# Optimization experiments

Measured on AMD Instinct MI355X. Metric: run time of the kernel, lower is better.

Reference implementation:

```python
import jax, jax.numpy as jnp
import numpy as np

N_NODES = 50000
N_EDGES = 800000
D_IN = 128
H1 = 128
H2 = 64
N_CLASSES = 4


def _sage_conv(x, src, dst, w_l, w_r, b, num_nodes):
    # PyG SAGEConv (aggr='mean'): out = lin_l(mean_{j->i} x_j) + lin_r(x_i)
    ones = jnp.ones((src.shape[0],), dtype=x.dtype)
    deg = jax.ops.segment_sum(ones, dst, num_segments=num_nodes)  # [N]
    agg = jax.ops.segment_sum(x[src], dst, num_segments=num_nodes)  # [N, d]
    agg = agg / jnp.maximum(deg, 1.0)[:, None]
    return agg @ w_l + b + x @ w_r


def setup_inputs() -> dict:
    key = jax.random.key(0)
    ks = jax.random.split(key, 12)
    x_content = jax.random.normal(ks[0], (N_NODES, D_IN), dtype=jnp.float32)
    edge_index = jax.random.randint(ks[1], (2, N_EDGES), 0, N_NODES, dtype=jnp.int32)
    edge_type = jax.random.randint(ks[2], (N_EDGES,), 0, 4, dtype=jnp.int32)
    s = 0.05
    params = {
        'w_l0': jax.random.normal(ks[3], (D_IN, H1), jnp.float32) * s,
        'w_r0': jax.random.normal(ks[4], (D_IN, H1), jnp.float32) * s,
        'b0': jnp.zeros((H1,), jnp.float32),
        'w_l1': jax.random.normal(ks[5], (H1, H1), jnp.float32) * s,
        'w_r1': jax.random.normal(ks[6], (H1, H1), jnp.float32) * s,
        'b1': jnp.zeros((H1,), jnp.float32),
        'w_l2': jax.random.normal(ks[7], (H1, H2), jnp.float32) * s,
        'w_r2': jax.random.normal(ks[8], (H1, H2), jnp.float32) * s,
        'b2': jnp.zeros((H2,), jnp.float32),
        'w_out': jax.random.normal(ks[9], (H2, N_CLASSES), jnp.float32) * s,
        'b_out': jnp.zeros((N_CLASSES,), jnp.float32),
    }
    return {'x_content': x_content, 'edge_index': edge_index, 'edge_type': edge_type, **params}


def reference(x_content, edge_index, edge_type,
              w_l0, w_r0, b0, w_l1, w_r1, b1, w_l2, w_r2, b2, w_out, b_out):
    # eval mode: dropout is identity
    src, dst = edge_index[0], edge_index[1]
    n = x_content.shape[0]
    x = x_content
    for (wl, wr, b) in ((w_l0, w_r0, b0), (w_l1, w_r1, b1), (w_l2, w_r2, b2)):
        x = _sage_conv(x, src, dst, wl, wr, b, n)
        x = jax.nn.relu(x)
    return x @ w_out + b_out
```

## Files before the change

### kernel.cpp

```cpp
#include <hip/hip_runtime.h>
#include <hip/hip_fp16.h>

#define D 128

constexpr int RSH = 14;
constexpr int RSZ = 1 << RSH;
constexpr int NRANGE = 4;
constexpr int CSH = 15;
constexpr int CSZ = 1 << CSH;

using short8 = __attribute__((ext_vector_type(8))) short;
using f32x4 = __attribute__((ext_vector_type(4))) float;

__device__ inline void splitf(float v, unsigned short& h, unsigned short& l) {
    unsigned b = __float_as_uint(v);
    h = (unsigned short)(b >> 16);
    float fh = __uint_as_float(b & 0xffff0000u);
    float r = v - fh;
    l = (unsigned short)(__float_as_uint(r) >> 16);
}


__global__ __launch_bounds__(1024) void hist_rank(
    const int* __restrict__ dst, unsigned* __restrict__ hist,
    unsigned short* __restrict__ rank, int n_edges, int nchunk) {
    __shared__ unsigned lh[RSZ / 2];
    int b = blockIdx.x;
    int r = b & (NRANGE - 1), c = b >> 2;
    int t = threadIdx.x;
    for (int i = t; i < RSZ / 2; i += 1024) lh[i] = 0;
    __syncthreads();
    int e0 = c << CSH, e1 = min(n_edges, e0 + CSZ);
    for (int e = e0 + t; e < e1; e += 1024) {
        int d = dst[e];
        if ((d >> RSH) == r) {
            int ii = d & (RSZ - 1);
            unsigned sh = (ii & 1) * 16;
            unsigned old = atomicAdd(&lh[ii >> 1], 1u << sh);
            rank[e] = (unsigned short)((old >> sh) & 0xffffu);
        }
    }
    __syncthreads();
    unsigned* gh = hist + (size_t)(r * nchunk + c) * (RSZ / 2);
    for (int i = t; i < RSZ / 2; i += 1024) gh[i] = lh[i];
}

struct WSplitArgs {
    const float* src[6];
    unsigned short* dh[6];
    unsigned short* dl[6];
};

__global__ __launch_bounds__(256) void deg_splitw(
    const unsigned short* __restrict__ hist16, int* __restrict__ deg,
    int* __restrict__ partials, int n_nodes, int nchunk, int nblk, WSplitArgs a) {
    __shared__ int sd[256];
    int b = blockIdx.x, t = threadIdx.x;
    if (b >= nblk) {
        int g = (b - nblk) * 256 + t;
        int m, e, N;
        if (g < 65536) { m = g >> 14; e = g & 16383; N = 128; }
        else { int t2 = g - 65536; m = 4 + (t2 >> 13); e = t2 & 8191; N = 64; }
        int sh = (N == 128) ? 7 : 6;
        int k = e >> sh;
        int n = e & (N - 1);
        float v = a.src[m][e];
        unsigned short h, l;
        splitf(v, h, l);
        a.dh[m][n * 128 + k] = h;
        a.dl[m][n * 128 + k] = l;
        return;
    }
    int i = b * 256 + t;
    int s = 0;
    if (i < n_nodes) {
        int r = i >> RSH, ii = i & (RSZ - 1);
        const unsigned short* hp = hist16 + (size_t)r * nchunk * RSZ + ii;
        for (int c = 0; c < nchunk; ++c) s += hp[(size_t)c * RSZ];
        deg[i] = s;
    }
    sd[t] = s;
    __syncthreads();
    for (int st = 128; st > 0; st >>= 1) {
        if (t < st) sd[t] += sd[t + st];
        __syncthreads();
    }
    if (t == 0) partials[b] = sd[0];
}

__global__ __launch_bounds__(256) void scan_fill(
    const int* __restrict__ deg, const int* __restrict__ partials,
    const unsigned short* __restrict__ hist16, int* __restrict__ row_ptr,
    float* __restrict__ inv_deg, int* __restrict__ base,
    int n_nodes, int nchunk, int nblk) {
    __shared__ int sp[256];
    __shared__ int sd[256];
    int b = blockIdx.x, t = threadIdx.x;

    sp[t] = (t < b && t < nblk) ? partials[t] : 0;
    __syncthreads();
    for (int st = 128; st > 0; st >>= 1) {
        if (t < st) sp[t] += sp[t + st];
        __syncthreads();
    }
    int pbase = sp[0];

    int i = b * 256 + t;
    int v = (i < n_nodes) ? deg[i] : 0;
    sd[t] = v;
    __syncthreads();
    for (int d = 1; d < 256; d <<= 1) {
        int x = (t >= d) ? sd[t - d] : 0;
        __syncthreads();
        sd[t] += x;
        __syncthreads();
    }
    int excl = sd[t] - v + pbase;
    if (i < n_nodes) {
        row_ptr[i] = excl;
        int dv = v > 1 ? v : 1;
        inv_deg[i] = 1.0f / (float)dv;
        if (i == n_nodes - 1) row_ptr[n_nodes] = excl + v;
        int r = i >> RSH, ii = i & (RSZ - 1);
        int bacc = excl;
        for (int c = 0; c < nchunk; ++c) {
            size_t idx = (size_t)(r * nchunk + c) * RSZ + ii;
            base[idx] = bacc;
            bacc += hist16[idx];
        }
    }
}

__global__ __launch_bounds__(256) void fill_edges(
    const int* __restrict__ src, const int* __restrict__ dst,
    const unsigned short* __restrict__ rank, const int* __restrict__ base,
    int* __restrict__ csr, int n_edges, int nchunk) {
    int e = blockIdx.x * 256 + threadIdx.x;
    if (e >= n_edges) return;
    int d = dst[e];
    int c = e >> CSH;
    int r = d >> RSH;
    int slot = base[(size_t)(r * nchunk + c) * RSZ + (d & (RSZ - 1))] + rank[e];
    csr[slot] = src[e];
}

template <int BN, int NT, bool SPLITX>
__global__ __launch_bounds__(256) void gemm_lds(
    const float* __restrict__ X,
    const unsigned short* __restrict__ Ah, const unsigned short* __restrict__ Al,
    const unsigned short* __restrict__ W1h, const unsigned short* __restrict__ W1l,
    const unsigned short* __restrict__ W2h, const unsigned short* __restrict__ W2l,
    const float* __restrict__ bias, __half* __restrict__ P, float* __restrict__ Q, int M) {
    __shared__ short8 As[2][16 * 65];

    const int tid = threadIdx.x;
    const int wave = tid >> 6;
    const int lane = tid & 63;
    const int l15 = lane & 15;
    const int q = lane >> 4;
    const int m0 = blockIdx.x * 64;

    if constexpr (SPLITX) {
#pragma unroll
        for (int it = 0; it < 4; ++it) {
            int s = it * 256 + tid;
            int row = s >> 4, col16 = s & 15;
            int gr = min(m0 + row, M - 1);
            const float4* xp = (const float4*)X + (size_t)gr * 32 + col16 * 2;
            float4 v0 = xp[0], v1 = xp[1];
            float fv[8] = {v0.x, v0.y, v0.z, v0.w, v1.x, v1.y, v1.z, v1.w};
            short8 h, l;
#pragma unroll
            for (int j = 0; j < 8; ++j) {
                unsigned short hh_, ll_;
                splitf(fv[j], hh_, ll_);
                h[j] = (short)hh_;
                l[j] = (short)ll_;
            }
            As[0][col16 * 65 + row] = h;
            As[1][col16 * 65 + row] = l;
        }
    } else {
#pragma unroll
        for (int it = 0; it < 8; ++it) {
            int s = it * 256 + tid;
            int arr = s >> 10;
            int sp = s & 1023;
            int row = sp >> 4, col16 = sp & 15;
            int gr = min(m0 + row, M - 1);
            const unsigned short* src = (arr ? Al : Ah) + (size_t)gr * 128 + col16 * 8;
            As[arr][col16 * 65 + row] = *(const short8*)src;
        }
    }
    __syncthreads();

    const int isQ = wave >> 1;
    const int colbase = (wave & 1) * (NT * 16);
    const unsigned short* Wh = isQ ? W2h : W1h;
    const unsigned short* Wl = isQ ? W2l : W1l;

    float bvs[NT];
#pragma unroll
    for (int nt = 0; nt < NT; ++nt) bvs[nt] = isQ ? bias[colbase + nt * 16 + l15] : 0.f;

    f32x4 acc[4][NT] = {};

#pragma unroll 1
    for (int kt = 0; kt < 4; ++kt) {
        short8 Bh[NT], Bl[NT];
#pragma unroll
        for (int nt = 0; nt < NT; ++nt) {
            int c = colbase + nt * 16 + l15;
            int off = c * 128 + kt * 32 + q * 8;
            Bh[nt] = *(const short8*)(Wh + off);
            Bl[nt] = *(const short8*)(Wl + off);
        }
#pragma unroll
        for (int mt = 0; mt < 4; ++mt) {
            int ai = (kt * 4 + q) * 65 + mt * 16 + l15;
            short8 Afh = As[0][ai];
            short8 Afl = As[1][ai];
#pragma unroll
            for (int nt = 0; nt < NT; ++nt) {
                acc[mt][nt] = __builtin_amdgcn_mfma_f32_16x16x32_bf16(Afh, Bh[nt], acc[mt][nt], 0, 0, 0);
                acc[mt][nt] = __builtin_amdgcn_mfma_f32_16x16x32_bf16(Afh, Bl[nt], acc[mt][nt], 0, 0, 0);
                acc[mt][nt] = __builtin_amdgcn_mfma_f32_16x16x32_bf16(Afl, Bh[nt], acc[mt][nt], 0, 0, 0);
            }
        }
    }

#pragma unroll
    for (int mt = 0; mt < 4; ++mt) {
        int orow = m0 + mt * 16 + q * 4;
#pragma unroll
        for (int nt = 0; nt < NT; ++nt) {
            int col = colbase + nt * 16 + l15;
#pragma unroll
            for (int r = 0; r < 4; ++r) {
                int rr = orow + r;
                if (rr < M) {
                    if (isQ) Q[(size_t)rr * BN + col] = acc[mt][nt][r] + bvs[nt];
                    else P[(size_t)rr * BN + col] = __float2half(acc[mt][nt][r]);
                }
            }
        }
    }
}

__global__ __launch_bounds__(256) void agg_fused128(
    const __half* __restrict__ P, const float* __restrict__ Q,
    const int* __restrict__ row_ptr, const int* __restrict__ csr,
    const float* __restrict__ inv_deg, unsigned short* __restrict__ Hh,
    unsigned short* __restrict__ Hl, int n_nodes) {
    int node = (blockIdx.x * blockDim.x + threadIdx.x) >> 6;
    int lane = threadIdx.x & 63;
    if (node >= n_nodes) return;
    int beg = row_ptr[node], end = row_ptr[node + 1];
    const int g = lane >> 4;
    const int l = lane & 15;
    float a[2][8] = {};
    int e = beg;
    for (; e + 8 <= end; e += 8) {
#pragma unroll
        for (int j = 0; j < 2; ++j) {
            int s = csr[e + 4 * j + g];
            uint4 raw = *(const uint4*)(P + (size_t)s * 128 + l * 8);
            float2 f01 = __half22float2(*reinterpret_cast<__half2*>(&raw.x));
            float2 f23 = __half22float2(*reinterpret_cast<__half2*>(&raw.y));
            float2 f45 = __half22float2(*reinterpret_cast<__half2*>(&raw.z));
            float2 f67 = __half22float2(*reinterpret_cast<__half2*>(&raw.w));
            a[j][0] += f01.x; a[j][1] += f01.y; a[j][2] += f23.x; a[j][3] += f23.y;
            a[j][4] += f45.x; a[j][5] += f45.y; a[j][6] += f67.x; a[j][7] += f67.y;
        }
    }
    for (; e < end; e += 4) {
        int idx = e + g;
        if (idx < end) {
            int s = csr[idx];
            uint4 raw = *(const uint4*)(P + (size_t)s * 128 + l * 8);
            float2 f01 = __half22float2(*reinterpret_cast<__half2*>(&raw.x));
            float2 f23 = __half22float2(*reinterpret_cast<__half2*>(&raw.y));
            float2 f45 = __half22float2(*reinterpret_cast<__half2*>(&raw.z));
            float2 f67 = __half22float2(*reinterpret_cast<__half2*>(&raw.w));
            a[0][0] += f01.x; a[0][1] += f01.y; a[0][2] += f23.x; a[0][3] += f23.y;
            a[0][4] += f45.x; a[0][5] += f45.y; a[0][6] += f67.x; a[0][7] += f67.y;
        }
    }
    float s[8];
#pragma unroll
    for (int k = 0; k < 8; ++k) {
        s[k] = a[0][k] + a[1][k];
        s[k] += __shfl_xor(s[k], 16);
        s[k] += __shfl_xor(s[k], 32);
    }
    if (lane < 16) {
        float w = inv_deg[node];
        const float4* Q4 = (const float4*)Q;
        float4 q0 = Q4[(size_t)node * 32 + 2 * l];
        float4 q1 = Q4[(size_t)node * 32 + 2 * l + 1];
        float h0 = fmaxf(fmaf(s[0], w, q0.x), 0.f);
        float h1 = fmaxf(fmaf(s[1], w, q0.y), 0.f);
        float h2 = fmaxf(fmaf(s[2], w, q0.z), 0.f);
        float h3 = fmaxf(fmaf(s[3], w, q0.w), 0.f);
        float h4 = fmaxf(fmaf(s[4], w, q1.x), 0.f);
        float h5 = fmaxf(fmaf(s[5], w, q1.y), 0.f);
        float h6 = fmaxf(fmaf(s[6], w, q1.z), 0.f);
        float h7 = fmaxf(fmaf(s[7], w, q1.w), 0.f);
        ushort4 hv0, lv0, hv1, lv1;
        splitf(h0, hv0.x, lv0.x);
        splitf(h1, hv0.y, lv0.y);
        splitf(h2, hv0.z, lv0.z);
        splitf(h3, hv0.w, lv0.w);
        splitf(h4, hv1.x, lv1.x);
        splitf(h5, hv1.y, lv1.y);
        splitf(h6, hv1.z, lv1.z);
        splitf(h7, hv1.w, lv1.w);
        ((ushort4*)Hh)[(size_t)node * 32 + 2 * l] = hv0;
        ((ushort4*)Hh)[(size_t)node * 32 + 2 * l + 1] = hv1;
        ((ushort4*)Hl)[(size_t)node * 32 + 2 * l] = lv0;
        ((ushort4*)Hl)[(size_t)node * 32 + 2 * l + 1] = lv1;
    }
}

__global__ __launch_bounds__(256) void agg64_head(
    const __half* __restrict__ P, const float* __restrict__ Q,
    const int* __restrict__ row_ptr, const int* __restrict__ csr,
    const float* __restrict__ inv_deg, const float* __restrict__ Wo,
    const float* __restrict__ bo, float* __restrict__ out, int n_nodes) {
    int node = (blockIdx.x * blockDim.x + threadIdx.x) >> 6;
    int lane = threadIdx.x & 63;
    if (node >= n_nodes) return;
    int beg = row_ptr[node], end = row_ptr[node + 1];
    const int quarter = lane >> 4;
    const int l = lane & 15;
    float a[2][4] = {};
    int e = beg;
    for (; e + 8 <= end; e += 8) {
#pragma unroll
        for (int j = 0; j < 2; ++j) {
            int s = csr[e + 4 * j + quarter];
            uint2 raw = *(const uint2*)(P + (size_t)s * 64 + l * 4);
            float2 f01 = __half22float2(*reinterpret_cast<__half2*>(&raw.x));
            float2 f23 = __half22float2(*reinterpret_cast<__half2*>(&raw.y));
            a[j][0] += f01.x; a[j][1] += f01.y; a[j][2] += f23.x; a[j][3] += f23.y;
        }
    }
    for (; e < end; e += 4) {
        int idx = e + quarter;
        if (idx < end) {
            int s = csr[idx];
            uint2 raw = *(const uint2*)(P + (size_t)s * 64 + l * 4);
            float2 f01 = __half22float2(*reinterpret_cast<__half2*>(&raw.x));
            float2 f23 = __half22float2(*reinterpret_cast<__half2*>(&raw.y));
            a[0][0] += f01.x; a[0][1] += f01.y; a[0][2] += f23.x; a[0][3] += f23.y;
        }
    }
    float s0 = a[0][0] + a[1][0];
    float s1 = a[0][1] + a[1][1];
    float s2 = a[0][2] + a[1][2];
    float s3 = a[0][3] + a[1][3];
    s0 += __shfl_xor(s0, 16); s0 += __shfl_xor(s0, 32);
    s1 += __shfl_xor(s1, 16); s1 += __shfl_xor(s1, 32);
    s2 += __shfl_xor(s2, 16); s2 += __shfl_xor(s2, 32);
    s3 += __shfl_xor(s3, 16); s3 += __shfl_xor(s3, 32);
    if (lane < 16) {
        float w = inv_deg[node];
        float4 qv = ((const float4*)Q)[(size_t)node * 16 + l];
        float h0 = fmaxf(fmaf(s0, w, qv.x), 0.f);
        float h1 = fmaxf(fmaf(s1, w, qv.y), 0.f);
        float h2 = fmaxf(fmaf(s2, w, qv.z), 0.f);
        float h3 = fmaxf(fmaf(s3, w, qv.w), 0.f);
        const float4* Wo4 = (const float4*)Wo;
        float4 w0 = Wo4[4 * l + 0], w1 = Wo4[4 * l + 1], w2 = Wo4[4 * l + 2], w3 = Wo4[4 * l + 3];
        float c0 = h0 * w0.x + h1 * w1.x + h2 * w2.x + h3 * w3.x;
        float c1 = h0 * w0.y + h1 * w1.y + h2 * w2.y + h3 * w3.y;
        float c2 = h0 * w0.z + h1 * w1.z + h2 * w2.z + h3 * w3.z;
        float c3 = h0 * w0.w + h1 * w1.w + h2 * w2.w + h3 * w3.w;
#pragma unroll
        for (int m = 8; m > 0; m >>= 1) {
            c0 += __shfl_xor(c0, m);
            c1 += __shfl_xor(c1, m);
            c2 += __shfl_xor(c2, m);
            c3 += __shfl_xor(c3, m);
        }
        if (l == 0) {
            float4 r;
            r.x = c0 + bo[0];
            r.y = c1 + bo[1];
            r.z = c2 + bo[2];
            r.w = c3 + bo[3];
            ((float4*)out)[node] = r;
        }
    }
}

extern "C" void kernel_launch(void* const* d_in, const int* in_sizes, int n_in,
                              void* d_out, int out_size, void* d_ws, size_t ws_size,
                              hipStream_t stream) {
    const float* x = (const float*)d_in[0];
    const int* ei = (const int*)d_in[1];
    const float* wl0 = (const float*)d_in[3];
    const float* wr0 = (const float*)d_in[4];
    const float* b0 = (const float*)d_in[5];
    const float* wl1 = (const float*)d_in[6];
    const float* wr1 = (const float*)d_in[7];
    const float* b1 = (const float*)d_in[8];
    const float* wl2 = (const float*)d_in[9];
    const float* wr2 = (const float*)d_in[10];
    const float* b2 = (const float*)d_in[11];
    const float* wo = (const float*)d_in[12];
    const float* bo = (const float*)d_in[13];

    const int n_nodes = in_sizes[0] / D;
    const int n_edges = in_sizes[1] / 2;
    const int* srcp = ei;
    const int* dstp = ei + n_edges;

    char* ws = (char*)d_ws;
    size_t off = 0;
    auto carve = [&](size_t bytes) -> void* {
        void* p = ws + off;
        off = (off + bytes + 255) & ~(size_t)255;
        return p;
    };
    int* deg = (int*)carve((size_t)n_nodes * 4);
    int* row_ptr = (int*)carve((size_t)(n_nodes + 1) * 4);
    int* partials = (int*)carve(256 * 4);
    float* inv_deg = (float*)carve((size_t)n_nodes * 4);
    unsigned short* rankb = (unsigned short*)carve((size_t)n_edges * 2);
    int* csr = (int*)carve((size_t)n_edges * 4);
    __half* Pbuf = (__half*)carve((size_t)n_nodes * D * 2);
    float* Qbuf = (float*)carve((size_t)n_nodes * D * 4);
    unsigned short* hh = (unsigned short*)carve((size_t)n_nodes * D * 2);
    unsigned short* hl = (unsigned short*)carve((size_t)n_nodes * D * 2);
    unsigned short* wt = (unsigned short*)carve((size_t)(4 * 128 * 128 + 2 * 64 * 128) * 2 * 2);
    unsigned short* wl0h = wt;
    unsigned short* wl0l = wl0h + 128 * 128;
    unsigned short* wr0h = wl0l + 128 * 128;
    unsigned short* wr0l = wr0h + 128 * 128;
    unsigned short* wl1h = wr0l + 128 * 128;
    unsigned short* wl1l = wl1h + 128 * 128;
    unsigned short* wr1h = wl1l + 128 * 128;
    unsigned short* wr1l = wr1h + 128 * 128;
    unsigned short* wl2h = wr1l + 128 * 128;
    unsigned short* wl2l = wl2h + 64 * 128;
    unsigned short* wr2h = wl2l + 64 * 128;
    unsigned short* wr2l = wr2h + 64 * 128;

    const int nchunk = (n_edges + CSZ - 1) >> CSH;
    unsigned* hist = (unsigned*)Qbuf;
    unsigned short* hist16 = (unsigned short*)Qbuf;
    int* basep = (int*)Pbuf;

    const int nblk = (n_nodes + 255) / 256;
    const int wblocks = (4 * 128 * 128 + 2 * 64 * 128) / 256;

    WSplitArgs wa;
    wa.src[0] = wl0; wa.dh[0] = wl0h; wa.dl[0] = wl0l;
    wa.src[1] = wr0; wa.dh[1] = wr0h; wa.dl[1] = wr0l;
    wa.src[2] = wl1; wa.dh[2] = wl1h; wa.dl[2] = wl1l;
    wa.src[3] = wr1; wa.dh[3] = wr1h; wa.dl[3] = wr1l;
    wa.src[4] = wl2; wa.dh[4] = wl2h; wa.dl[4] = wl2l;
    wa.src[5] = wr2; wa.dh[5] = wr2h; wa.dl[5] = wr2l;

    hist_rank<<<NRANGE * nchunk, 1024, 0, stream>>>(dstp, hist, rankb, n_edges, nchunk);
    deg_splitw<<<nblk + wblocks, 256, 0, stream>>>(hist16, deg, partials, n_nodes, nchunk, nblk, wa);
    scan_fill<<<nblk, 256, 0, stream>>>(deg, partials, hist16, row_ptr, inv_deg, basep,
                                        n_nodes, nchunk, nblk);
    fill_edges<<<(n_edges + 255) / 256, 256, 0, stream>>>(srcp, dstp, rankb, basep, csr,
                                                          n_edges, nchunk);

    const int agg_blocks = (n_nodes * 64 + 255) / 256;
    const int gemm_blocks = (n_nodes + 63) / 64;

    gemm_lds<128, 4, true><<<gemm_blocks, 256, 0, stream>>>(
        x, nullptr, nullptr, wl0h, wl0l, wr0h, wr0l, b0, Pbuf, Qbuf, n_nodes);
    agg_fused128<<<agg_blocks, 256, 0, stream>>>(Pbuf, Qbuf, row_ptr, csr, inv_deg, hh, hl, n_nodes);
    gemm_lds<128, 4, false><<<gemm_blocks, 256, 0, stream>>>(
        nullptr, hh, hl, wl1h, wl1l, wr1h, wr1l, b1, Pbuf, Qbuf, n_nodes);
    agg_fused128<<<agg_blocks, 256, 0, stream>>>(Pbuf, Qbuf, row_ptr, csr, inv_deg, hh, hl, n_nodes);
    gemm_lds<64, 2, false><<<gemm_blocks, 256, 0, stream>>>(
        nullptr, hh, hl, wl2h, wl2l, wr2h, wr2l, b2, Pbuf, Qbuf, n_nodes);
    agg64_head<<<agg_blocks, 256, 0, stream>>>(Pbuf, Qbuf, row_ptr, csr, inv_deg,
                                               wo, bo, (float*)d_out, n_nodes);
}
```

Measured before the change: 306.5 us.

## Co-schedule histogram with layer-0 GEMM and prefetch CSR indices in aggregation

Merges the edge histogram/rank kernel and the first-layer GEMM into one launch, with block ranges selecting the role. This lets the atomic-bound histogram work overlap the compute-bound X projection, and it needs separate hist/base buffers instead of aliasing P/Q. Weight splitting becomes its own small kernel ahead of both, degree summation is split out, and the GEMM path uses 1024-thread blocks with one 16-column tile per wave. The aggregation loops also software-prefetch the next CSR indices to hide index-load latency. The costs are extra memory for the new buffers, an extra launch, and a different GEMM tiling in layer 0.

```diff
diff --git a/kernel.cpp b/kernel.cpp
--- a/kernel.cpp
+++ b/kernel.cpp
@@ -20,57 +20,132 @@
     l = (unsigned short)(__float_as_uint(r) >> 16);
 }
 
-
-__global__ __launch_bounds__(1024) void hist_rank(
-    const int* __restrict__ dst, unsigned* __restrict__ hist,
-    unsigned short* __restrict__ rank, int n_edges, int nchunk) {
-    __shared__ unsigned lh[RSZ / 2];
-    int b = blockIdx.x;
-    int r = b & (NRANGE - 1), c = b >> 2;
-    int t = threadIdx.x;
-    for (int i = t; i < RSZ / 2; i += 1024) lh[i] = 0;
-    __syncthreads();
-    int e0 = c << CSH, e1 = min(n_edges, e0 + CSZ);
-    for (int e = e0 + t; e < e1; e += 1024) {
-        int d = dst[e];
-        if ((d >> RSH) == r) {
-            int ii = d & (RSZ - 1);
-            unsigned sh = (ii & 1) * 16;
-            unsigned old = atomicAdd(&lh[ii >> 1], 1u << sh);
-            rank[e] = (unsigned short)((old >> sh) & 0xffffu);
-        }
-    }
-    __syncthreads();
-    unsigned* gh = hist + (size_t)(r * nchunk + c) * (RSZ / 2);
-    for (int i = t; i < RSZ / 2; i += 1024) gh[i] = lh[i];
-}
-
 struct WSplitArgs {
     const float* src[6];
     unsigned short* dh[6];
     unsigned short* dl[6];
+    int n[6];
 };
 
-__global__ __launch_bounds__(256) void deg_splitw(
+__global__ __launch_bounds__(256) void split_w(WSplitArgs a) {
+    int m = blockIdx.y;
+    int N = a.n[m];
+    int e = blockIdx.x * 256 + threadIdx.x;
+    if (e >= 128 * N) return;
+    int sh = (N == 128) ? 7 : 6;
+    int k = e >> sh;
+    int n = e & (N - 1);
+    float v = a.src[m][e];
+    unsigned short h, l;
+    splitf(v, h, l);
+    a.dh[m][n * 128 + k] = h;
+    a.dl[m][n * 128 + k] = l;
+}
+
+__global__ __launch_bounds__(1024) void hist_gemm_x(
+    const int* __restrict__ dst, unsigned* __restrict__ hist,
+    unsigned short* __restrict__ rank, int n_edges, int nchunk, int nhist,
+    const float* __restrict__ X,
+    const unsigned short* __restrict__ W1h, const unsigned short* __restrict__ W1l,
+    const unsigned short* __restrict__ W2h, const unsigned short* __restrict__ W2l,
+    const float* __restrict__ bias, __half* __restrict__ P, float* __restrict__ Q, int M) {
+    __shared__ __align__(16) char smem[2 * 16 * 65 * 16];
+
+    const int b = blockIdx.x;
+    const int tid = threadIdx.x;
+
+    if (b < nhist) {
+        unsigned* lh = (unsigned*)smem;
+        int r = b & (NRANGE - 1), c = b >> 2;
+        for (int i = tid; i < RSZ / 2; i += 1024) lh[i] = 0;
+        __syncthreads();
+        int e0 = c << CSH, e1 = min(n_edges, e0 + CSZ);
+        for (int e = e0 + tid; e < e1; e += 1024) {
+            int d = dst[e];
+            if ((d >> RSH) == r) {
+                int ii = d & (RSZ - 1);
+                unsigned sh = (ii & 1) * 16;
+                unsigned old = atomicAdd(&lh[ii >> 1], 1u << sh);
+                rank[e] = (unsigned short)((old >> sh) & 0xffffu);
+            }
+        }
+        __syncthreads();
+        unsigned* gh = hist + (size_t)(r * nchunk + c) * (RSZ / 2);
+        for (int i = tid; i < RSZ / 2; i += 1024) gh[i] = lh[i];
+        return;
+    }
+
+    short8(*As)[16 * 65] = (short8(*)[16 * 65])smem;
+    const int wave = tid >> 6;
+    const int lane = tid & 63;
+    const int l15 = lane & 15;
+    const int q = lane >> 4;
+    const int m0 = (b - nhist) * 64;
+
+    {
+        int row = tid >> 4, col16 = tid & 15;
+        int gr = min(m0 + row, M - 1);
+        const float4* xp = (const float4*)X + (size_t)gr * 32 + col16 * 2;
+        float4 v0 = xp[0], v1 = xp[1];
+        float fv[8] = {v0.x, v0.y, v0.z, v0.w, v1.x, v1.y, v1.z, v1.w};
+        short8 h, l;
+#pragma unroll
+        for (int j = 0; j < 8; ++j) {
+            unsigned short hh_, ll_;
+            splitf(fv[j], hh_, ll_);
+            h[j] = (short)hh_;
+            l[j] = (short)ll_;
+        }
+        As[0][col16 * 65 + row] = h;
+        As[1][col16 * 65 + row] = l;
+    }
+    __syncthreads();
+
+    const int isQ = wave >> 3;
+    const int colbase = (wave & 7) * 16;
+    const unsigned short* Wh = isQ ? W2h : W1h;
+    const unsigned short* Wl = isQ ? W2l : W1l;
+    const float bv = isQ ? bias[colbase + l15] : 0.f;
+
+    f32x4 acc[4] = {};
+
+#pragma unroll 1
+    for (int kt = 0; kt < 4; ++kt) {
+        int c = colbase + l15;
+        int woff = c * 128 + kt * 32 + q * 8;
+        short8 Bh = *(const short8*)(Wh + woff);
+        short8 Bl = *(const short8*)(Wl + woff);
+#pragma unroll
+        for (int mt = 0; mt < 4; ++mt) {
+            int ai = (kt * 4 + q) * 65 + mt * 16 + l15;
+            short8 Afh = As[0][ai];
+            short8 Afl = As[1][ai];
+            acc[mt] = __builtin_amdgcn_mfma_f32_16x16x32_bf16(Afh, Bh, acc[mt], 0, 0, 0);
+            acc[mt] = __builtin_amdgcn_mfma_f32_16x16x32_bf16(Afh, Bl, acc[mt], 0, 0, 0);
+            acc[mt] = __builtin_amdgcn_mfma_f32_16x16x32_bf16(Afl, Bh, acc[mt], 0, 0, 0);
+        }
+    }
+
+#pragma unroll
+    for (int mt = 0; mt < 4; ++mt) {
+        int orow = m0 + mt * 16 + q * 4;
+        int col = colbase + l15;
+#pragma unroll
+        for (int r = 0; r < 4; ++r) {
+            int rr = orow + r;
+            if (rr < M) {
+                if (isQ) Q[(size_t)rr * 128 + col] = acc[mt][r] + bv;
+                else P[(size_t)rr * 128 + col] = __float2half(acc[mt][r]);
+            }
+        }
+    }
+}
+
+__global__ __launch_bounds__(256) void deg_sum_partials(
     const unsigned short* __restrict__ hist16, int* __restrict__ deg,
-    int* __restrict__ partials, int n_nodes, int nchunk, int nblk, WSplitArgs a) {
+    int* __restrict__ partials, int n_nodes, int nchunk) {
     __shared__ int sd[256];
     int b = blockIdx.x, t = threadIdx.x;
-    if (b >= nblk) {
-        int g = (b - nblk) * 256 + t;
-        int m, e, N;
-        if (g < 65536) { m = g >> 14; e = g & 16383; N = 128; }
-        else { int t2 = g - 65536; m = 4 + (t2 >> 13); e = t2 & 8191; N = 64; }
-        int sh = (N == 128) ? 7 : 6;
-        int k = e >> sh;
-        int n = e & (N - 1);
-        float v = a.src[m][e];
-        unsigned short h, l;
-        splitf(v, h, l);
-        a.dh[m][n * 128 + k] = h;
-        a.dl[m][n * 128 + k] = l;
-        return;
-    }
     int i = b * 256 + t;
     int s = 0;
     if (i < n_nodes) {
@@ -144,9 +219,8 @@
     csr[slot] = src[e];
 }
 
-template <int BN, int NT, bool SPLITX>
+template <int BN, int NT>
 __global__ __launch_bounds__(256) void gemm_lds(
-    const float* __restrict__ X,
     const unsigned short* __restrict__ Ah, const unsigned short* __restrict__ Al,
     const unsigned short* __restrict__ W1h, const unsigned short* __restrict__ W1l,
     const unsigned short* __restrict__ W2h, const unsigned short* __restrict__ W2l,
@@ -160,37 +234,15 @@
     const int q = lane >> 4;
     const int m0 = blockIdx.x * 64;
 
-    if constexpr (SPLITX) {
-#pragma unroll
-        for (int it = 0; it < 4; ++it) {
-            int s = it * 256 + tid;
-            int row = s >> 4, col16 = s & 15;
-            int gr = min(m0 + row, M - 1);
-            const float4* xp = (const float4*)X + (size_t)gr * 32 + col16 * 2;
-            float4 v0 = xp[0], v1 = xp[1];
-            float fv[8] = {v0.x, v0.y, v0.z, v0.w, v1.x, v1.y, v1.z, v1.w};
-            short8 h, l;
-#pragma unroll
-            for (int j = 0; j < 8; ++j) {
-                unsigned short hh_, ll_;
-                splitf(fv[j], hh_, ll_);
-                h[j] = (short)hh_;
-                l[j] = (short)ll_;
-            }
-            As[0][col16 * 65 + row] = h;
-            As[1][col16 * 65 + row] = l;
-        }
-    } else {
-#pragma unroll
-        for (int it = 0; it < 8; ++it) {
-            int s = it * 256 + tid;
-            int arr = s >> 10;
-            int sp = s & 1023;
-            int row = sp >> 4, col16 = sp & 15;
-            int gr = min(m0 + row, M - 1);
-            const unsigned short* src = (arr ? Al : Ah) + (size_t)gr * 128 + col16 * 8;
-            As[arr][col16 * 65 + row] = *(const short8*)src;
-        }
+#pragma unroll
+    for (int it = 0; it < 8; ++it) {
+        int s = it * 256 + tid;
+        int arr = s >> 10;
+        int sp = s & 1023;
+        int row = sp >> 4, col16 = sp & 15;
+        int gr = min(m0 + row, M - 1);
+        const unsigned short* src = (arr ? Al : Ah) + (size_t)gr * 128 + col16 * 8;
+        As[arr][col16 * 65 + row] = *(const short8*)src;
     }
     __syncthreads();
 
@@ -260,11 +312,18 @@
     const int l = lane & 15;
     float a[2][8] = {};
     int e = beg;
-    for (; e + 8 <= end; e += 8) {
+    bool have = (e + 8 <= end);
+    int i0 = 0, i1 = 0;
+    if (have) { i0 = csr[e + g]; i1 = csr[e + 4 + g]; }
+    while (have) {
+        int en = e + 8;
+        bool hn = (en + 8 <= end);
+        int n0 = 0, n1 = 0;
+        if (hn) { n0 = csr[en + g]; n1 = csr[en + 4 + g]; }
+        int ss[2] = {i0, i1};
 #pragma unroll
         for (int j = 0; j < 2; ++j) {
-            int s = csr[e + 4 * j + g];
-            uint4 raw = *(const uint4*)(P + (size_t)s * 128 + l * 8);
+            uint4 raw = *(const uint4*)(P + (size_t)ss[j] * 128 + l * 8);
             float2 f01 = __half22float2(*reinterpret_cast<__half2*>(&raw.x));
             float2 f23 = __half22float2(*reinterpret_cast<__half2*>(&raw.y));
             float2 f45 = __half22float2(*reinterpret_cast<__half2*>(&raw.z));
@@ -272,6 +331,7 @@
             a[j][0] += f01.x; a[j][1] += f01.y; a[j][2] += f23.x; a[j][3] += f23.y;
             a[j][4] += f45.x; a[j][5] += f45.y; a[j][6] += f67.x; a[j][7] += f67.y;
         }
+        e = en; i0 = n0; i1 = n1; have = hn;
     }
     for (; e < end; e += 4) {
         int idx = e + g;
@@ -335,15 +395,23 @@
     const int l = lane & 15;
     float a[2][4] = {};
     int e = beg;
-    for (; e + 8 <= end; e += 8) {
+    bool have = (e + 8 <= end);
+    int i0 = 0, i1 = 0;
+    if (have) { i0 = csr[e + quarter]; i1 = csr[e + 4 + quarter]; }
+    while (have) {
+        int en = e + 8;
+        bool hn = (en + 8 <= end);
+        int n0 = 0, n1 = 0;
+        if (hn) { n0 = csr[en + quarter]; n1 = csr[en + 4 + quarter]; }
+        int ss[2] = {i0, i1};
 #pragma unroll
         for (int j = 0; j < 2; ++j) {
-            int s = csr[e + 4 * j + quarter];
-            uint2 raw = *(const uint2*)(P + (size_t)s * 64 + l * 4);
+            uint2 raw = *(const uint2*)(P + (size_t)ss[j] * 64 + l * 4);
             float2 f01 = __half22float2(*reinterpret_cast<__half2*>(&raw.x));
             float2 f23 = __half22float2(*reinterpret_cast<__half2*>(&raw.y));
             a[j][0] += f01.x; a[j][1] += f01.y; a[j][2] += f23.x; a[j][3] += f23.y;
         }
+        e = en; i0 = n0; i1 = n1; have = hn;
     }
     for (; e < end; e += 4) {
         int idx = e + quarter;
@@ -448,39 +516,38 @@
     unsigned short* wr2l = wr2h + 64 * 128;
 
     const int nchunk = (n_edges + CSZ - 1) >> CSH;
-    unsigned* hist = (unsigned*)Qbuf;
-    unsigned short* hist16 = (unsigned short*)Qbuf;
-    int* basep = (int*)Pbuf;
+    unsigned* hist = (unsigned*)carve((size_t)NRANGE * nchunk * (RSZ / 2) * 4);
+    unsigned short* hist16 = (unsigned short*)hist;
+    int* basep = (int*)carve((size_t)NRANGE * nchunk * RSZ * 4);
 
     const int nblk = (n_nodes + 255) / 256;
-    const int wblocks = (4 * 128 * 128 + 2 * 64 * 128) / 256;
+    const int nhist = NRANGE * nchunk;
+    const int gemm_blocks = (n_nodes + 63) / 64;
+    const int agg_blocks = (n_nodes * 64 + 255) / 256;
 
     WSplitArgs wa;
-    wa.src[0] = wl0; wa.dh[0] = wl0h; wa.dl[0] = wl0l;
-    wa.src[1] = wr0; wa.dh[1] = wr0h; wa.dl[1] = wr0l;
-    wa.src[2] = wl1; wa.dh[2] = wl1h; wa.dl[2] = wl1l;
-    wa.src[3] = wr1; wa.dh[3] = wr1h; wa.dl[3] = wr1l;
-    wa.src[4] = wl2; wa.dh[4] = wl2h; wa.dl[4] = wl2l;
-    wa.src[5] = wr2; wa.dh[5] = wr2h; wa.dl[5] = wr2l;
-
-    hist_rank<<<NRANGE * nchunk, 1024, 0, stream>>>(dstp, hist, rankb, n_edges, nchunk);
-    deg_splitw<<<nblk + wblocks, 256, 0, stream>>>(hist16, deg, partials, n_nodes, nchunk, nblk, wa);
+    wa.src[0] = wl0; wa.dh[0] = wl0h; wa.dl[0] = wl0l; wa.n[0] = 128;
+    wa.src[1] = wr0; wa.dh[1] = wr0h; wa.dl[1] = wr0l; wa.n[1] = 128;
+    wa.src[2] = wl1; wa.dh[2] = wl1h; wa.dl[2] = wl1l; wa.n[2] = 128;
+    wa.src[3] = wr1; wa.dh[3] = wr1h; wa.dl[3] = wr1l; wa.n[3] = 128;
+    wa.src[4] = wl2; wa.dh[4] = wl2h; wa.dl[4] = wl2l; wa.n[4] = 64;
+    wa.src[5] = wr2; wa.dh[5] = wr2h; wa.dl[5] = wr2l; wa.n[5] = 64;
+
+    split_w<<<dim3(64, 6), 256, 0, stream>>>(wa);
+    hist_gemm_x<<<nhist + gemm_blocks, 1024, 0, stream>>>(
+        dstp, hist, rankb, n_edges, nchunk, nhist,
+        x, wl0h, wl0l, wr0h, wr0l, b0, Pbuf, Qbuf, n_nodes);
+    deg_sum_partials<<<nblk, 256, 0, stream>>>(hist16, deg, partials, n_nodes, nchunk);
     scan_fill<<<nblk, 256, 0, stream>>>(deg, partials, hist16, row_ptr, inv_deg, basep,
                                         n_nodes, nchunk, nblk);
     fill_edges<<<(n_edges + 255) / 256, 256, 0, stream>>>(srcp, dstp, rankb, basep, csr,
                                                           n_edges, nchunk);
-
-    const int agg_blocks = (n_nodes * 64 + 255) / 256;
-    const int gemm_blocks = (n_nodes + 63) / 64;
-
-    gemm_lds<128, 4, true><<<gemm_blocks, 256, 0, stream>>>(
-        x, nullptr, nullptr, wl0h, wl0l, wr0h, wr0l, b0, Pbuf, Qbuf, n_nodes);
     agg_fused128<<<agg_blocks, 256, 0, stream>>>(Pbuf, Qbuf, row_ptr, csr, inv_deg, hh, hl, n_nodes);
-    gemm_lds<128, 4, false><<<gemm_blocks, 256, 0, stream>>>(
-        nullptr, hh, hl, wl1h, wl1l, wr1h, wr1l, b1, Pbuf, Qbuf, n_nodes);
+    gemm_lds<128, 4><<<gemm_blocks, 256, 0, stream>>>(
+        hh, hl, wl1h, wl1l, wr1h, wr1l, b1, Pbuf, Qbuf, n_nodes);
     agg_fused128<<<agg_blocks, 256, 0, stream>>>(Pbuf, Qbuf, row_ptr, csr, inv_deg, hh, hl, n_nodes);
-    gemm_lds<64, 2, false><<<gemm_blocks, 256, 0, stream>>>(
-        nullptr, hh, hl, wl2h, wl2l, wr2h, wr2l, b2, Pbuf, Qbuf, n_nodes);
+    gemm_lds<64, 2><<<gemm_blocks, 256, 0, stream>>>(
+        hh, hl, wl2h, wl2l, wr2h, wr2l, b2, Pbuf, Qbuf, n_nodes);
     agg64_head<<<agg_blocks, 256, 0, stream>>>(Pbuf, Qbuf, row_ptr, csr, inv_deg,
                                                wo, bo, (float*)d_out, n_nodes);
 }
```

After: 289.8 us. -5.4%, faster.
